# Optimization experiments

Hardware: AMD Instinct MI355X
Metric: run time of the kernel (lower is better)

Reference implementation:

```python
import jax, jax.numpy as jnp
import numpy as np

N = 100000      # nodes
E = 1600000     # edges
G = 1024        # graphs in batch
H = 128         # graph_hidden
F_IN = 38
DEPTH = 4
EPS = 1e-5


def setup_inputs() -> dict:
    key = jax.random.key(0)
    ks = jax.random.split(key, 16)
    inp = {
        "h": jax.random.normal(ks[0], (N, F_IN), jnp.float32),
        "src": jax.random.randint(ks[1], (E,), 0, N, jnp.int32),
        "dst": jax.random.randint(ks[2], (E,), 0, N, jnp.int32),
        "node2graph": jnp.sort(jax.random.randint(ks[3], (N,), 0, G, jnp.int32)),
        "W1": jax.random.normal(ks[4], (F_IN, H), jnp.float32) * 0.1,
        "b1": jnp.zeros((H,), jnp.float32),
        "g1": jnp.ones((H,), jnp.float32),
        "be1": jnp.zeros((H,), jnp.float32),
        "W2s": jax.random.normal(ks[5], (DEPTH - 1, H, H), jnp.float32) * 0.1,
        "b2s": jnp.zeros((DEPTH - 1, H), jnp.float32),
        "g2s": jnp.ones((DEPTH - 1, H), jnp.float32),
        "be2s": jnp.zeros((DEPTH - 1, H), jnp.float32),
        "aw": jax.random.normal(ks[6], (H, 1), jnp.float32) * 0.1,
        "ab": jnp.zeros((1,), jnp.float32),
        "Wf1": jax.random.normal(ks[7], (H, 512), jnp.float32) * 0.1,
        "bf1": jnp.zeros((512,), jnp.float32),
        "gf1": jnp.ones((512,), jnp.float32),
        "bef1": jnp.zeros((512,), jnp.float32),
        "Wl": jax.random.normal(ks[8], (512, 256), jnp.float32) * 0.05,
        "bl": jnp.zeros((256,), jnp.float32),
        "gl": jnp.ones((256,), jnp.float32),
        "bel": jnp.zeros((256,), jnp.float32),
        "Wf2": jax.random.normal(ks[9], (256, 67), jnp.float32) * 0.05,
        "bf2": jnp.zeros((67,), jnp.float32),
    }
    return inp


def _bn(x, g, b):
    # BatchNorm1d in training mode: batch stats (biased variance), eps=1e-5.
    m = jnp.mean(x, axis=0)
    v = jnp.mean(jnp.square(x - m), axis=0)
    return g * (x - m) * jax.lax.rsqrt(v + EPS) + b


def reference(h, src, dst, node2graph,
              W1, b1, g1, be1, W2s, b2s, g2s, be2s,
              aw, ab, Wf1, bf1, gf1, bef1, Wl, bl, gl, bel, Wf2, bf2):
    ones_e = jnp.ones((E,), h.dtype)
    deg_out = jax.ops.segment_sum(ones_e, src, num_segments=N)
    deg_in = jax.ops.segment_sum(ones_e, dst, num_segments=N)
    ns = jax.lax.rsqrt(jnp.maximum(deg_out, 1.0))  # src-side D^{-1/2}
    nd = jax.lax.rsqrt(jnp.maximum(deg_in, 1.0))   # dst-side D^{-1/2}

    def gconv(x, W, b):
        # DGL GraphConv norm='both': D_dst^{-1/2} A D_src^{-1/2} x W + b
        msg = (x * ns[:, None])[src]                      # [E, F] gather
        agg = jax.ops.segment_sum(msg, dst, num_segments=N)
        return (agg * nd[:, None]) @ W + b

    # dropout p = 0.0 -> identity
    x = jax.nn.relu(_bn(gconv(h, W1, b1), g1, be1))
    for i in range(DEPTH - 1):
        x = jax.nn.relu(_bn(gconv(x, W2s[i], b2s[i]), g2s[i], be2s[i]))

    # WeightAndSum readout: sigmoid-gated segment sum over nodes per graph
    atom_weights = x @ aw + ab                            # [N, 1] (pre-sigmoid, returned)
    w = jax.nn.sigmoid(atom_weights)
    hg = jax.ops.segment_sum(x * w, node2graph, num_segments=G)  # [G, H]

    y = jax.nn.relu(_bn(hg @ Wf1 + bf1, gf1, bef1))
    y = jax.nn.relu(_bn(y @ Wl + bl, gl, bel))
    y = jax.nn.sigmoid(y @ Wf2 + bf2)                     # [G, 67]
    return (y, atom_weights)
```

## Files before the change

### kernel.cpp

```cpp
#include <hip/hip_runtime.h>
#include <math.h>

#define NN 100000
#define NE 1600000
#define NG 1024
#define MAXDEG 64
#define EPSB 1e-5f

#define NBUK 1563
#define NBLK 256
#define EPB  6250
#define FLAT (2*NBUK*NBLK)
#define NCH  ((FLAT + 1023)/1024)

typedef _Float16 h16;
typedef __attribute__((ext_vector_type(2))) _Float16 h16x2;
typedef __attribute__((ext_vector_type(4))) _Float16 h16x4;
typedef __attribute__((ext_vector_type(8))) _Float16 h16x8;
typedef __attribute__((ext_vector_type(4))) float f32x4;

static __device__ __forceinline__ float sigmoidf_(float x){ return 1.f/(1.f+__expf(-x)); }

__global__ __launch_bounds__(512)
void k_hist(const int* __restrict__ src, const int* __restrict__ dst,
            int* __restrict__ blockHist){
  __shared__ int hd[NBUK];
  __shared__ int hs[NBUK];
  int b = blockIdx.x, t = threadIdx.x;
  for (int j = t; j < NBUK; j += 512){ hd[j] = 0; hs[j] = 0; }
  __syncthreads();
  int e0 = b*EPB, e1 = e0 + EPB;
  for (int i = e0 + t; i < e1; i += 512){
    atomicAdd(&hd[dst[i]>>6], 1);
    atomicAdd(&hs[src[i]>>6], 1);
  }
  __syncthreads();
  for (int j = t; j < NBUK; j += 512){
    blockHist[(size_t)j*NBLK + b] = hd[j];
    blockHist[(size_t)(NBUK + j)*NBLK + b] = hs[j];
  }
}

__global__ __launch_bounds__(256)
void k_scan1(int* __restrict__ data, int* __restrict__ csum){
  __shared__ int s[256];
  int blk = blockIdx.x, t = threadIdx.x;
  int base = blk*1024 + t*4;
  int v0=0,v1=0,v2=0,v3=0;
  if (base+0 < FLAT) v0 = data[base+0];
  if (base+1 < FLAT) v1 = data[base+1];
  if (base+2 < FLAT) v2 = data[base+2];
  if (base+3 < FLAT) v3 = data[base+3];
  int tot = v0+v1+v2+v3;
  s[t] = tot; __syncthreads();
  for (int o=1;o<256;o<<=1){ int x = (t>=o)? s[t-o]:0; __syncthreads(); s[t]+=x; __syncthreads(); }
  int excl = s[t] - tot;
  if (t == 255) csum[blk] = s[255];
  if (base+0 < FLAT) data[base+0] = excl;
  if (base+1 < FLAT) data[base+1] = excl + v0;
  if (base+2 < FLAT) data[base+2] = excl + v0 + v1;
  if (base+3 < FLAT) data[base+3] = excl + v0 + v1 + v2;
}

__global__ void k_scan2(int* __restrict__ csum){
  __shared__ int s[1024];
  int t = threadIdx.x;
  int x = (t < NCH) ? csum[t] : 0;
  s[t] = x; __syncthreads();
  for (int o=1;o<1024;o<<=1){ int y = (t>=o)? s[t-o]:0; __syncthreads(); s[t]+=y; __syncthreads(); }
  if (t < NCH) csum[t] = s[t] - x;
}

static __device__ __forceinline__ int rd_scanned(const int* data, const int* csum, int idx){
  return data[idx] + csum[idx >> 10];
}

__global__ __launch_bounds__(512)
void k_scatter(const int* __restrict__ src, const int* __restrict__ dst,
               const int* __restrict__ scanned, const int* __restrict__ csum,
               unsigned int* __restrict__ sortedBuf){
  __shared__ int bd[NBUK];
  __shared__ int bs[NBUK];
  int b = blockIdx.x, t = threadIdx.x;
  for (int j = t; j < NBUK; j += 512){
    bd[j] = rd_scanned(scanned, csum, j*NBLK + b);
    bs[j] = rd_scanned(scanned, csum, (NBUK + j)*NBLK + b);
  }
  __syncthreads();
  int e0 = b*EPB, e1 = e0 + EPB;
  for (int i = e0 + t; i < e1; i += 512){
    int s = src[i], d = dst[i];
    int posD = atomicAdd(&bd[d>>6], 1);
    sortedBuf[posD] = (unsigned int)s | ((unsigned int)(d & 63) << 20);
    int posS = atomicAdd(&bs[s>>6], 1);
    sortedBuf[posS] = (unsigned int)s;
  }
}

__global__ __launch_bounds__(256)
void k_build(const unsigned int* __restrict__ sortedBuf, const int* __restrict__ scanned,
             const int* __restrict__ csum, const float* __restrict__ h,
             int* __restrict__ eidx, int* __restrict__ degI,
             h16* __restrict__ nsh, float* __restrict__ nd, h16* __restrict__ hn){
  __shared__ int cnt[64];
  __shared__ float nsl[64];
  int k = blockIdx.x, t = threadIdx.x;
  int v0 = k*64;
  int nv = NN - v0; if (nv > 64) nv = 64;
  if (t < 64) cnt[t] = 0;
  __syncthreads();
  int startD = rd_scanned(scanned, csum, k*NBLK);
  int endD   = rd_scanned(scanned, csum, (k+1)*NBLK);
  for (int i = startD + t; i < endD; i += 256){
    unsigned int u = sortedBuf[i];
    int lid = (int)(u >> 20);
    int slot = atomicAdd(&cnt[lid], 1);
    if (slot < MAXDEG) eidx[(size_t)(v0 + lid)*MAXDEG + slot] = (int)(u & 0xFFFFFu);
  }
  __syncthreads();
  if (t < nv){
    int v = v0 + t;
    int dI = cnt[t];
    degI[v] = dI;
    nd[v] = rsqrtf(fmaxf((float)dI, 1.f));
    int c = dI > MAXDEG ? MAXDEG : dI;
    int ad = (c + 7) & ~7; if (ad < 8) ad = 8; if (ad > MAXDEG) ad = MAXDEG;
    for (int i = c; i < ad; i++) eidx[(size_t)v*MAXDEG + i] = NN;
  }
  __syncthreads();
  if (t < 64) cnt[t] = 0;
  __syncthreads();
  int startS = rd_scanned(scanned, csum, (NBUK + k)*NBLK);
  int endS   = (k+1 < NBUK) ? rd_scanned(scanned, csum, (NBUK + k + 1)*NBLK) : 2*NE;
  for (int i = startS + t; i < endS; i += 256){
    atomicAdd(&cnt[sortedBuf[i] & 63u], 1);
  }
  __syncthreads();
  if (t < 64){
    float nsv = 0.f;
    if (t < nv){
      nsv = rsqrtf(fmaxf((float)cnt[t], 1.f));
      nsh[v0 + t] = (h16)nsv;
    }
    nsl[t] = nsv;
  }
  __syncthreads();
  for (int i = t; i < 64*64; i += 256){
    int r = i >> 6, c = i & 63;
    int v = v0 + r;
    if (v < NN){
      float val = (c < 38) ? h[(size_t)v*38 + c]*nsl[r] : 0.f;
      hn[(size_t)v*64 + c] = (h16)val;
    }
  }
  if (k == 0){
    for (int i = t; i < 64; i += 256) hn[(size_t)NN*64 + i] = (h16)0.f;
  }
}

__global__ void k_prepg(const int* __restrict__ n2g,
                        int* __restrict__ gs, int* __restrict__ ge, float* __restrict__ stats,
                        h16* __restrict__ nsh, h16* __restrict__ XA, h16* __restrict__ XB){
  int v = blockIdx.x*256 + threadIdx.x;
  if (v < NN){
    int g = n2g[v];
    if (v == 0){
      for (int q = 0; q <= g; q++) gs[q] = 0;
      for (int q = 0; q < g; q++) ge[q] = 0;
    } else {
      int gp = n2g[v-1];
      if (gp != g){
        for (int q = gp+1; q <= g; q++) gs[q] = v;
        for (int q = gp; q < g; q++) ge[q] = v;
      }
    }
    if (v == NN-1){
      for (int q = g+1; q < NG; q++) gs[q] = NN;
      for (int q = g; q < NG; q++) ge[q] = NN;
    }
  }
  if (v == NN) nsh[NN] = (h16)0.f;
  if (blockIdx.x == 0){
    int t = threadIdx.x;
    for (int j = t; j < 4096; j += 256) stats[j] = 0.f;
    if (t < 128){ XA[(size_t)NN*128 + t] = (h16)0.f; XB[(size_t)NN*128 + t] = (h16)0.f; }
  }
}

__global__ void k_convall(const float* __restrict__ W1, const float* __restrict__ W2s,
                          const float* __restrict__ Wf1, const float* __restrict__ Wl,
                          h16* __restrict__ W1t, h16* __restrict__ W2t,
                          h16* __restrict__ Wf1t, h16* __restrict__ Wlt){
  int i = blockIdx.x*256 + threadIdx.x;
  if (i < 8192){
    int c = i >> 6, k = i & 63;
    W1t[i] = (k < 38) ? (h16)W1[(size_t)k*128 + c] : (h16)0.f;
  } else if (i < 57344){
    int j = i - 8192; int l = j >> 14; int r = j & 16383;
    int c = r >> 7, k = r & 127;
    W2t[j] = (h16)W2s[(size_t)l*16384 + (size_t)k*128 + c];
  } else if (i < 122880){
    int j = i - 57344; int c = j >> 7, k = j & 127;
    Wf1t[j] = (h16)Wf1[(size_t)k*512 + c];
  } else if (i < 253952){
    int j = i - 122880; int c = j >> 9, k = j & 511;
    Wlt[j] = (h16)Wl[(size_t)k*256 + c];
  }
}

__global__ __launch_bounds__(256)
void k_gs40(const h16* __restrict__ hn, const int* __restrict__ eidx,
            const int* __restrict__ degI, const float* __restrict__ nd,
            h16* __restrict__ A38){
  int v = (blockIdx.x*256 + threadIdx.x) >> 6;
  int lane = threadIdx.x & 63;
  if (v >= NN) return;
  int deg = degI[v]; if (deg > MAXDEG) deg = MAXDEG;
  int deg8 = (deg + 7) & ~7; if (deg8 < 8) deg8 = 8; if (deg8 > MAXDEG) deg8 = MAXDEG;
  const int* row = eidx + (size_t)v*MAXDEG;
  int g = lane / 20;
  int c0 = 2*(lane % 20);
  bool act = (lane < 40);
  int gg = g & 1;
  float a0 = 0.f, a1 = 0.f;
  int4 s4 = *(const int4*)(row + 4*gg);
  h16x2 u0={}, u1={}, u2={}, u3={};
  if (act){
    u0 = *(const h16x2*)(hn + (size_t)s4.x*64 + c0);
    u1 = *(const h16x2*)(hn + (size_t)s4.y*64 + c0);
    u2 = *(const h16x2*)(hn + (size_t)s4.z*64 + c0);
    u3 = *(const h16x2*)(hn + (size_t)s4.w*64 + c0);
  }
  for (int e = 0; e < deg8; e += 8){
    int nx = (e + 8 < deg8) ? e + 8 : e;
    int4 s4n = *(const int4*)(row + nx + 4*gg);
    h16x2 n0={}, n1={}, n2={}, n3={};
    if (act){
      n0 = *(const h16x2*)(hn + (size_t)s4n.x*64 + c0);
      n1 = *(const h16x2*)(hn + (size_t)s4n.y*64 + c0);
      n2 = *(const h16x2*)(hn + (size_t)s4n.z*64 + c0);
      n3 = *(const h16x2*)(hn + (size_t)s4n.w*64 + c0);
    }
    a0 += ((float)u0[0] + (float)u1[0]) + ((float)u2[0] + (float)u3[0]);
    a1 += ((float)u0[1] + (float)u1[1]) + ((float)u2[1] + (float)u3[1]);
    u0=n0; u1=n1; u2=n2; u3=n3;
  }
  float b0 = __shfl(a0, lane + 20);
  float b1 = __shfl(a1, lane + 20);
  if (lane < 20){
    float ndv = nd[v];
    h16x2 o; o[0] = (h16)((a0 + b0)*ndv); o[1] = (h16)((a1 + b1)*ndv);
    *(h16x2*)(A38 + (size_t)v*64 + c0) = o;
  } else if (lane < 32){
    h16x2 o; o[0] = (h16)0.f; o[1] = (h16)0.f;
    *(h16x2*)(A38 + (size_t)v*64 + 40 + 2*(lane - 20)) = o;
  }
}

__global__ __launch_bounds__(256)
void k_gs128(const h16* __restrict__ X, const int* __restrict__ eidx,
             const int* __restrict__ degI, const h16* __restrict__ nsh,
             const float* __restrict__ nd, const float* __restrict__ stats,
             const float* __restrict__ gam, const float* __restrict__ bet,
             h16* __restrict__ agg){
  __shared__ float scs[128], shs[128];
  int t = threadIdx.x;
  if (t < 128){
    float m = stats[t]*(1.f/(float)NN);
    float var = fmaxf(stats[128+t]*(1.f/(float)NN) - m*m, 0.f);
    float inv = rsqrtf(var + EPSB);
    float sc = gam[t]*inv;
    scs[t] = sc; shs[t] = fmaf(-sc, m, bet[t]);
  }
  __syncthreads();
  int v = (blockIdx.x*256 + t) >> 6;
  int lane = t & 63;
  if (v >= NN) return;
  int deg = degI[v]; if (deg > MAXDEG) deg = MAXDEG;
  int deg8 = (deg + 7) & ~7; if (deg8 < 8) deg8 = 8; if (deg8 > MAXDEG) deg8 = MAXDEG;
  const int* row = eidx + (size_t)v*MAXDEG;
  int half = lane >> 5;
  int c0 = 4*(lane & 31);
  h16x2 scp0, scp1, shp0, shp1, za;
  za[0] = (h16)0.f; za[1] = (h16)0.f;
  scp0[0]=(h16)scs[c0];   scp0[1]=(h16)scs[c0+1];
  scp1[0]=(h16)scs[c0+2]; scp1[1]=(h16)scs[c0+3];
  shp0[0]=(h16)shs[c0];   shp0[1]=(h16)shs[c0+1];
  shp1[0]=(h16)shs[c0+2]; shp1[1]=(h16)shs[c0+3];
  h16x2 acA0=za, acA1=za, acB0=za, acB1=za;
  int4 s4 = *(const int4*)(row + 4*half);
  h16 w0=nsh[s4.x], w1=nsh[s4.y], w2=nsh[s4.z], w3=nsh[s4.w];
  uint2 x0 = *(const uint2*)(X + (size_t)s4.x*128 + c0);
  uint2 x1 = *(const uint2*)(X + (size_t)s4.y*128 + c0);
  uint2 x2 = *(const uint2*)(X + (size_t)s4.z*128 + c0);
  uint2 x3 = *(const uint2*)(X + (size_t)s4.w*128 + c0);
  for (int e = 0; e < deg8; e += 8){
    int nx = (e + 8 < deg8) ? e + 8 : e;
    int4 s4n = *(const int4*)(row + nx + 4*half);
    h16 v0n=nsh[s4n.x], v1n=nsh[s4n.y], v2n=nsh[s4n.z], v3n=nsh[s4n.w];
    uint2 y0 = *(const uint2*)(X + (size_t)s4n.x*128 + c0);
    uint2 y1 = *(const uint2*)(X + (size_t)s4n.y*128 + c0);
    uint2 y2 = *(const uint2*)(X + (size_t)s4n.z*128 + c0);
    uint2 y3 = *(const uint2*)(X + (size_t)s4n.w*128 + c0);
    h16x2 np, pa, pb;
    np[0]=w0; np[1]=w0;
    pa = __builtin_bit_cast(h16x2, x0.x);
    pb = __builtin_bit_cast(h16x2, x0.y);
    pa = __builtin_elementwise_max(__builtin_elementwise_fma(pa, scp0, shp0), za);
    pb = __builtin_elementwise_max(__builtin_elementwise_fma(pb, scp1, shp1), za);
    acA0 = __builtin_elementwise_fma(pa, np, acA0);
    acA1 = __builtin_elementwise_fma(pb, np, acA1);
    np[0]=w1; np[1]=w1;
    pa = __builtin_bit_cast(h16x2, x1.x);
    pb = __builtin_bit_cast(h16x2, x1.y);
    pa = __builtin_elementwise_max(__builtin_elementwise_fma(pa, scp0, shp0), za);
    pb = __builtin_elementwise_max(__builtin_elementwise_fma(pb, scp1, shp1), za);
    acB0 = __builtin_elementwise_fma(pa, np, acB0);
    acB1 = __builtin_elementwise_fma(pb, np, acB1);
    np[0]=w2; np[1]=w2;
    pa = __builtin_bit_cast(h16x2, x2.x);
    pb = __builtin_bit_cast(h16x2, x2.y);
    pa = __builtin_elementwise_max(__builtin_elementwise_fma(pa, scp0, shp0), za);
    pb = __builtin_elementwise_max(__builtin_elementwise_fma(pb, scp1, shp1), za);
    acA0 = __builtin_elementwise_fma(pa, np, acA0);
    acA1 = __builtin_elementwise_fma(pb, np, acA1);
    np[0]=w3; np[1]=w3;
    pa = __builtin_bit_cast(h16x2, x3.x);
    pb = __builtin_bit_cast(h16x2, x3.y);
    pa = __builtin_elementwise_max(__builtin_elementwise_fma(pa, scp0, shp0), za);
    pb = __builtin_elementwise_max(__builtin_elementwise_fma(pb, scp1, shp1), za);
    acB0 = __builtin_elementwise_fma(pa, np, acB0);
    acB1 = __builtin_elementwise_fma(pb, np, acB1);
    x0=y0; x1=y1; x2=y2; x3=y3;
    w0=v0n; w1=v1n; w2=v2n; w3=v3n;
  }
  float a0 = (float)acA0[0] + (float)acB0[0];
  float a1 = (float)acA0[1] + (float)acB0[1];
  float a2 = (float)acA1[0] + (float)acB1[0];
  float a3 = (float)acA1[1] + (float)acB1[1];
  a0 += __shfl_xor(a0, 32);
  a1 += __shfl_xor(a1, 32);
  a2 += __shfl_xor(a2, 32);
  a3 += __shfl_xor(a3, 32);
  if (half == 0){
    float ndv = nd[v];
    h16x4 o;
    o[0] = (h16)(a0*ndv); o[1] = (h16)(a1*ndv);
    o[2] = (h16)(a2*ndv); o[3] = (h16)(a3*ndv);
    *(h16x4*)(agg + (size_t)v*128 + c0) = o;
  }
}

__global__ __launch_bounds__(256)
void k_mgemm(const h16* __restrict__ A, const h16* __restrict__ Wt,
             const float* __restrict__ bias, h16* __restrict__ Cout,
             float* __restrict__ stats, int M, int K, int Nc){
  __shared__ h16 As[128][72];
  __shared__ h16 Bs[128][72];
  __shared__ float sred[2][128];
  int m0 = blockIdx.x*128, n0 = blockIdx.y*128;
  int t = threadIdx.x, w = t>>6, lane = t&63;
  int wr = (w>>1)*64, wc = (w&1)*64;
  f32x4 acc[4][4] = {};

  int ar = t>>3;
  int ac = (t&7)*8;
  for (int k0=0; k0<K; k0+=64){
    #pragma unroll
    for (int rr=0; rr<128; rr+=32){
      int gm = m0 + ar + rr;
      h16x8 val = {};
      if (gm < M) val = *(const h16x8*)(A + (size_t)gm*K + k0 + ac);
      *(h16x8*)&As[ar+rr][ac] = val;
    }
    #pragma unroll
    for (int rr=0; rr<128; rr+=32){
      int gc = n0 + ar + rr;
      h16x8 val = {};
      if (gc < Nc) val = *(const h16x8*)(Wt + (size_t)gc*K + k0 + ac);
      *(h16x8*)&Bs[ar+rr][ac] = val;
    }
    __syncthreads();
    int rsel = lane & 15;
    #pragma unroll
    for (int kk=0; kk<64; kk+=32){
      int ksel = kk + (lane>>4)*8;
      h16x8 af[4], bfr[4];
      #pragma unroll
      for (int i=0;i<4;i++) af[i]  = *(const h16x8*)&As[wr + i*16 + rsel][ksel];
      #pragma unroll
      for (int j=0;j<4;j++) bfr[j] = *(const h16x8*)&Bs[wc + j*16 + rsel][ksel];
      #pragma unroll
      for (int i=0;i<4;i++)
        #pragma unroll
        for (int j=0;j<4;j++)
          acc[i][j] = __builtin_amdgcn_mfma_f32_16x16x32_f16(af[i], bfr[j], acc[i][j], 0, 0, 0);
    }
    __syncthreads();
  }

  float csum[4] = {}, csq[4] = {};
  int colsel = lane & 15, rowsel = (lane>>4)*4;
  #pragma unroll
  for (int j=0;j<4;j++){
    int gc = n0 + wc + j*16 + colsel;
    float bv = (gc < Nc) ? bias[gc] : 0.f;
    #pragma unroll
    for (int i=0;i<4;i++){
      #pragma unroll
      for (int r=0;r<4;r++){
        int gm = m0 + wr + i*16 + rowsel + r;
        if (gm < M && gc < Nc){
          float v = acc[i][j][r] + bv;
          Cout[(size_t)gm*Nc + gc] = (h16)v;
          csum[j] += v; csq[j] += v*v;
        }
      }
    }
  }
  if (stats){
    ((float*)sred)[t] = 0.f;
    __syncthreads();
    #pragma unroll
    for (int j=0;j<4;j++){
      int lc = wc + j*16 + colsel;
      atomicAdd(&sred[0][lc], csum[j]);
      atomicAdd(&sred[1][lc], csq[j]);
    }
    __syncthreads();
    if (t < 128){
      int gc = n0 + t;
      if (gc < Nc){
        atomicAdd(&stats[gc],      sred[0][t]);
        atomicAdd(&stats[Nc + gc], sred[1][t]);
      }
    }
  }
}

__global__ __launch_bounds__(256)
void k_mgemmbn(const h16* __restrict__ A, const h16* __restrict__ Wt,
               const float* __restrict__ bias, h16* __restrict__ Cout,
               float* __restrict__ statsOut, const float* __restrict__ statsIn,
               const float* __restrict__ gam, const float* __restrict__ bet,
               float invM, int M, int K, int Nc){
  __shared__ float scs[512], shs[512];
  __shared__ h16 As[128][72];
  __shared__ h16 Bs[128][72];
  __shared__ float sred[2][128];
  int t = threadIdx.x;
  for (int c = t; c < K; c += 256){
    float m = statsIn[c]*invM;
    float var = fmaxf(statsIn[K+c]*invM - m*m, 0.f);
    float inv = rsqrtf(var + EPSB);
    float sc = gam[c]*inv;
    scs[c] = sc; shs[c] = fmaf(-sc, m, bet[c]);
  }
  __syncthreads();
  int m0 = blockIdx.x*128, n0 = blockIdx.y*128;
  int w = t>>6, lane = t&63;
  int wr = (w>>1)*64, wc = (w&1)*64;
  f32x4 acc[4][4] = {};

  int ar = t>>3;
  int ac = (t&7)*8;
  for (int k0=0; k0<K; k0+=64){
    #pragma unroll
    for (int rr=0; rr<128; rr+=32){
      int gm = m0 + ar + rr;
      h16x8 val = {};
      if (gm < M){
        h16x8 raw = *(const h16x8*)(A + (size_t)gm*K + k0 + ac);
        #pragma unroll
        for (int j=0;j<8;j++){
          int kk = k0 + ac + j;
          val[j] = (h16)fmaxf(fmaf((float)raw[j], scs[kk], shs[kk]), 0.f);
        }
      }
      *(h16x8*)&As[ar+rr][ac] = val;
    }
    #pragma unroll
    for (int rr=0; rr<128; rr+=32){
      int gc = n0 + ar + rr;
      h16x8 val = {};
      if (gc < Nc) val = *(const h16x8*)(Wt + (size_t)gc*K + k0 + ac);
      *(h16x8*)&Bs[ar+rr][ac] = val;
    }
    __syncthreads();
    int rsel = lane & 15;
    #pragma unroll
    for (int kk=0; kk<64; kk+=32){
      int ksel = kk + (lane>>4)*8;
      h16x8 af[4], bfr[4];
      #pragma unroll
      for (int i=0;i<4;i++) af[i]  = *(const h16x8*)&As[wr + i*16 + rsel][ksel];
      #pragma unroll
      for (int j=0;j<4;j++) bfr[j] = *(const h16x8*)&Bs[wc + j*16 + rsel][ksel];
      #pragma unroll
      for (int i=0;i<4;i++)
        #pragma unroll
        for (int j=0;j<4;j++)
          acc[i][j] = __builtin_amdgcn_mfma_f32_16x16x32_f16(af[i], bfr[j], acc[i][j], 0, 0, 0);
    }
    __syncthreads();
  }

  float csum[4] = {}, csq[4] = {};
  int colsel = lane & 15, rowsel = (lane>>4)*4;
  #pragma unroll
  for (int j=0;j<4;j++){
    int gc = n0 + wc + j*16 + colsel;
    float bv = (gc < Nc) ? bias[gc] : 0.f;
    #pragma unroll
    for (int i=0;i<4;i++){
      #pragma unroll
      for (int r=0;r<4;r++){
        int gm = m0 + wr + i*16 + rowsel + r;
        if (gm < M && gc < Nc){
          float v = acc[i][j][r] + bv;
          Cout[(size_t)gm*Nc + gc] = (h16)v;
          csum[j] += v; csq[j] += v*v;
        }
      }
    }
  }
  ((float*)sred)[t] = 0.f;
  __syncthreads();
  #pragma unroll
  for (int j=0;j<4;j++){
    int lc = wc + j*16 + colsel;
    atomicAdd(&sred[0][lc], csum[j]);
    atomicAdd(&sred[1][lc], csq[j]);
  }
  __syncthreads();
  if (t < 128){
    int gc = n0 + t;
    if (gc < Nc){
      atomicAdd(&statsOut[gc],      sred[0][t]);
      atomicAdd(&statsOut[Nc + gc], sred[1][t]);
    }
  }
}

__global__ __launch_bounds__(256)
void k_readout(const h16* __restrict__ X, const float* __restrict__ stats,
               const float* __restrict__ gam, const float* __restrict__ bet,
               const float* __restrict__ aw, const float* __restrict__ ab,
               const int* __restrict__ gs, const int* __restrict__ ge,
               float* __restrict__ awout, h16* __restrict__ hg){
  __shared__ float scs[128], shs[128], awv[128];
  __shared__ float red[4][128];
  int t = threadIdx.x;
  if (t < 128){
    float m = stats[t]*(1.f/(float)NN);
    float var = fmaxf(stats[128+t]*(1.f/(float)NN) - m*m, 0.f);
    float inv = rsqrtf(var + EPSB);
    float sc = gam[t]*inv;
    scs[t] = sc; shs[t] = fmaf(-sc, m, bet[t]);
    awv[t] = aw[t];
  }
  __syncthreads();
  int g = blockIdx.x;
  int s = gs[g], e = ge[g];
  int w = t>>6, lane = t&63, c0 = 2*lane;
  float sc0=scs[c0], sc1=scs[c0+1], sh0=shs[c0], sh1=shs[c0+1];
  float aw0=awv[c0], aw1=awv[c0+1];
  float ab0 = ab[0];
  float acc0=0.f, acc1=0.f;
  for (int n = s + w; n < e; n += 4){
    h16x2 u = *(const h16x2*)(X + (size_t)n*128 + c0);
    float x0 = fmaxf(fmaf((float)u[0], sc0, sh0), 0.f);
    float x1 = fmaxf(fmaf((float)u[1], sc1, sh1), 0.f);
    float d = x0*aw0 + x1*aw1;
    #pragma unroll
    for (int o=32;o>0;o>>=1) d += __shfl_xor(d, o);
    float tv = d + ab0;
    if (lane == 0) awout[n] = tv;
    float wn = sigmoidf_(tv);
    acc0 = fmaf(x0, wn, acc0);
    acc1 = fmaf(x1, wn, acc1);
  }
  red[w][c0] = acc0; red[w][c0+1] = acc1;
  __syncthreads();
  if (w == 0){
    float a0 = red[0][c0] + red[1][c0] + red[2][c0] + red[3][c0];
    float a1 = red[0][c0+1] + red[1][c0+1] + red[2][c0+1] + red[3][c0+1];
    h16x2 o; o[0] = (h16)a0; o[1] = (h16)a1;
    *(h16x2*)(hg + (size_t)g*128 + c0) = o;
  }
}

__global__ __launch_bounds__(256)
void k_finalbn(const h16* __restrict__ y2p, const float* __restrict__ Wf2,
               const float* __restrict__ bf2v, const float* __restrict__ statsIn,
               const float* __restrict__ gam, const float* __restrict__ bet,
               float* __restrict__ out){
  __shared__ float scs[256], shs[256];
  int t = threadIdx.x;
  {
    float m = statsIn[t]*(1.f/(float)NG);
    float var = fmaxf(statsIn[256+t]*(1.f/(float)NG) - m*m, 0.f);
    float inv = rsqrtf(var + EPSB);
    float sc = gam[t]*inv;
    scs[t] = sc; shs[t] = fmaf(-sc, m, bet[t]);
  }
  __syncthreads();
  int idx = blockIdx.x*256 + t;
  if (idx >= NG*67) return;
  int g = idx / 67, c = idx % 67;
  float s = bf2v[c];
  const h16* row = y2p + (size_t)g*256;
  for (int k=0;k<256;k+=2){
    h16x2 u = *(const h16x2*)(row + k);
    float x0 = fmaxf(fmaf((float)u[0], scs[k],   shs[k]),   0.f);
    float x1 = fmaxf(fmaf((float)u[1], scs[k+1], shs[k+1]), 0.f);
    s = fmaf(x0, Wf2[(size_t)k*67 + c], s);
    s = fmaf(x1, Wf2[(size_t)(k+1)*67 + c], s);
  }
  out[(size_t)g*67 + c] = sigmoidf_(s);
}

extern "C" void kernel_launch(void* const* d_in, const int* in_sizes, int n_in,
                              void* d_out, int out_size, void* d_ws, size_t ws_size,
                              hipStream_t stream){
  const float* h   = (const float*)d_in[0];
  const int*   src = (const int*)d_in[1];
  const int*   dst = (const int*)d_in[2];
  const int*   n2g = (const int*)d_in[3];
  const float* W1  = (const float*)d_in[4];
  const float* b1  = (const float*)d_in[5];
  const float* g1  = (const float*)d_in[6];
  const float* be1 = (const float*)d_in[7];
  const float* W2s = (const float*)d_in[8];
  const float* b2s = (const float*)d_in[9];
  const float* g2s = (const float*)d_in[10];
  const float* be2s= (const float*)d_in[11];
  const float* aw  = (const float*)d_in[12];
  const float* ab  = (const float*)d_in[13];
  const float* Wf1 = (const float*)d_in[14];
  const float* bf1 = (const float*)d_in[15];
  const float* gf1 = (const float*)d_in[16];
  const float* bef1= (const float*)d_in[17];
  const float* Wl  = (const float*)d_in[18];
  const float* bl  = (const float*)d_in[19];
  const float* gl  = (const float*)d_in[20];
  const float* bel = (const float*)d_in[21];
  const float* Wf2 = (const float*)d_in[22];
  const float* bf2v= (const float*)d_in[23];
  float* out = (float*)d_out;

  char* p = (char*)d_ws;
  auto carve = [&](size_t bytes)->void*{
    void* r = (void*)p; p += (bytes + 255) & ~(size_t)255; return r;
  };
  h16* XA   = (h16*)carve((size_t)(NN+1)*128*2);
  h16* XB   = (h16*)carve((size_t)(NN+1)*128*2);
  h16* hn   = (h16*)carve((size_t)(NN+1)*64*2);
  h16* A38  = (h16*)carve((size_t)NN*64*2);
  int* eidx = (int*)carve((size_t)NN*MAXDEG*4);
  unsigned int* sortedBuf = (unsigned int*)carve((size_t)2*NE*4);
  int* blockHist = (int*)carve((size_t)FLAT*4);
  int* csum = (int*)carve(1024*4);
  int* degI = (int*)carve((size_t)NN*4);
  h16* nsh = (h16*)carve((size_t)(NN+1)*2);
  float* nd = (float*)carve((size_t)NN*4);
  int* gsge = (int*)carve((size_t)2*NG*4);
  h16* hg   = (h16*)carve((size_t)NG*128*2);
  h16* y1p  = (h16*)carve((size_t)NG*512*2);
  h16* y2p  = (h16*)carve((size_t)NG*256*2);
  float* stats = (float*)carve(4096*4);
  h16* W1t  = (h16*)carve((size_t)128*64*2);
  h16* W2t  = (h16*)carve((size_t)3*128*128*2);
  h16* Wf1t = (h16*)carve((size_t)512*128*2);
  h16* Wlt  = (h16*)carve((size_t)256*512*2);

  int* gs = gsge;
  int* ge = gsge + NG;
  float* st1  = stats;
  float* st2a = stats + 256;
  float* st2b = stats + 512;
  float* st2c = stats + 768;
  float* stf1 = stats + 1024;
  float* stl  = stats + 2048;
  float* st2[3] = { st2a, st2b, st2c };

  k_convall<<<(253952+255)/256, 256, 0, stream>>>(W1, W2s, Wf1, Wl, W1t, W2t, Wf1t, Wlt);
  k_prepg  <<<(NN+1+255)/256, 256, 0, stream>>>(n2g, gs, ge, stats, nsh, XA, XB);

  k_hist   <<<NBLK, 512, 0, stream>>>(src, dst, blockHist);
  k_scan1  <<<NCH, 256, 0, stream>>>(blockHist, csum);
  k_scan2  <<<1, 1024, 0, stream>>>(csum);
  k_scatter<<<NBLK, 512, 0, stream>>>(src, dst, blockHist, csum, sortedBuf);
  k_build  <<<NBUK, 256, 0, stream>>>(sortedBuf, blockHist, csum, h, eidx, degI, nsh, nd, hn);

  const int nodeBlocks = (NN + 3)/4;
  const int gemmBlocks = (NN + 127)/128;

  k_gs40 <<<nodeBlocks, 256, 0, stream>>>(hn, eidx, degI, nd, A38);
  k_mgemm<<<dim3(gemmBlocks,1), 256, 0, stream>>>(A38, W1t, b1, XA, st1, NN, 64, 128);

  const float* stPrev[3] = { st1, st2a, st2b };
  const float* gPrev[3]  = { g1, g2s, g2s + 128 };
  const float* bePrev[3] = { be1, be2s, be2s + 128 };
  for (int i=0;i<3;i++){
    k_gs128<<<nodeBlocks, 256, 0, stream>>>(XA, eidx, degI, nsh, nd,
                                            stPrev[i], gPrev[i], bePrev[i], XB);
    k_mgemm<<<dim3(gemmBlocks,1), 256, 0, stream>>>(XB, W2t + (size_t)i*128*128, b2s + i*128,
                                                    XA, st2[i], NN, 128, 128);
  }

  k_readout<<<NG, 256, 0, stream>>>(XA, st2c, g2s + 256, be2s + 256, aw, ab,
                                    gs, ge, out + (size_t)NG*67, hg);

  k_mgemm  <<<dim3(NG/128, 4), 256, 0, stream>>>(hg, Wf1t, bf1, y1p, stf1, NG, 128, 512);
  k_mgemmbn<<<dim3(NG/128, 2), 256, 0, stream>>>(y1p, Wlt, bl, y2p, stl, stf1, gf1, bef1,
                                                 1.0f/(float)NG, NG, 512, 256);
  k_finalbn<<<(NG*67+255)/256, 256, 0, stream>>>(y2p, Wf2, bf2v, stl, gl, bel, out);
}
```

Measured before the change: 647.2 us.

## Load GEMM A-fragments directly from global memory and merge init kernels

The MFMA GEMM kernels (plain and BN-fused) stop staging the A tile in shared memory. Each wave now loads its A fragments straight from global memory into registers, applying the BN affine and ReLU per fragment in the fused variant, while only the weight tile still goes through LDS. The aim is to remove an LDS round trip and shared-memory footprint for A, which is used by a single wave anyway. The trade-off is less coalesced global loads and possibly redundant loads across the wave pairs that share rows. Separately, the weight-conversion and graph-prep kernels are merged into one launch to save a kernel launch.

Measured after the change: 634.8 us. About the same (-1.9%).

```diff
diff --git a/kernel.cpp b/kernel.cpp
--- a/kernel.cpp
+++ b/kernel.cpp
@@ -158,39 +158,13 @@
   }
 }
 
-__global__ void k_prepg(const int* __restrict__ n2g,
-                        int* __restrict__ gs, int* __restrict__ ge, float* __restrict__ stats,
-                        h16* __restrict__ nsh, h16* __restrict__ XA, h16* __restrict__ XB){
-  int v = blockIdx.x*256 + threadIdx.x;
-  if (v < NN){
-    int g = n2g[v];
-    if (v == 0){
-      for (int q = 0; q <= g; q++) gs[q] = 0;
-      for (int q = 0; q < g; q++) ge[q] = 0;
-    } else {
-      int gp = n2g[v-1];
-      if (gp != g){
-        for (int q = gp+1; q <= g; q++) gs[q] = v;
-        for (int q = gp; q < g; q++) ge[q] = v;
-      }
-    }
-    if (v == NN-1){
-      for (int q = g+1; q < NG; q++) gs[q] = NN;
-      for (int q = g; q < NG; q++) ge[q] = NN;
-    }
-  }
-  if (v == NN) nsh[NN] = (h16)0.f;
-  if (blockIdx.x == 0){
-    int t = threadIdx.x;
-    for (int j = t; j < 4096; j += 256) stats[j] = 0.f;
-    if (t < 128){ XA[(size_t)NN*128 + t] = (h16)0.f; XB[(size_t)NN*128 + t] = (h16)0.f; }
-  }
-}
-
-__global__ void k_convall(const float* __restrict__ W1, const float* __restrict__ W2s,
-                          const float* __restrict__ Wf1, const float* __restrict__ Wl,
-                          h16* __restrict__ W1t, h16* __restrict__ W2t,
-                          h16* __restrict__ Wf1t, h16* __restrict__ Wlt){
+__global__ void k_init(const float* __restrict__ W1, const float* __restrict__ W2s,
+                       const float* __restrict__ Wf1, const float* __restrict__ Wl,
+                       h16* __restrict__ W1t, h16* __restrict__ W2t,
+                       h16* __restrict__ Wf1t, h16* __restrict__ Wlt,
+                       const int* __restrict__ n2g, int* __restrict__ gs, int* __restrict__ ge,
+                       float* __restrict__ stats, h16* __restrict__ nsh,
+                       h16* __restrict__ XA, h16* __restrict__ XB){
   int i = blockIdx.x*256 + threadIdx.x;
   if (i < 8192){
     int c = i >> 6, k = i & 63;
@@ -205,6 +179,30 @@
   } else if (i < 253952){
     int j = i - 122880; int c = j >> 9, k = j & 511;
     Wlt[j] = (h16)Wl[(size_t)k*256 + c];
+  }
+  int v = i;
+  if (v < NN){
+    int g = n2g[v];
+    if (v == 0){
+      for (int q = 0; q <= g; q++) gs[q] = 0;
+      for (int q = 0; q < g; q++) ge[q] = 0;
+    } else {
+      int gp = n2g[v-1];
+      if (gp != g){
+        for (int q = gp+1; q <= g; q++) gs[q] = v;
+        for (int q = gp; q < g; q++) ge[q] = v;
+      }
+    }
+    if (v == NN-1){
+      for (int q = g+1; q < NG; q++) gs[q] = NN;
+      for (int q = g; q < NG; q++) ge[q] = NN;
+    }
+  }
+  if (v == NN) nsh[NN] = (h16)0.f;
+  if (blockIdx.x == 0){
+    int t = threadIdx.x;
+    for (int j = t; j < 4096; j += 256) stats[j] = 0.f;
+    if (t < 128){ XA[(size_t)NN*128 + t] = (h16)0.f; XB[(size_t)NN*128 + t] = (h16)0.f; }
   }
 }
 
@@ -355,41 +353,42 @@
 void k_mgemm(const h16* __restrict__ A, const h16* __restrict__ Wt,
              const float* __restrict__ bias, h16* __restrict__ Cout,
              float* __restrict__ stats, int M, int K, int Nc){
-  __shared__ h16 As[128][72];
   __shared__ h16 Bs[128][72];
   __shared__ float sred[2][128];
   int m0 = blockIdx.x*128, n0 = blockIdx.y*128;
   int t = threadIdx.x, w = t>>6, lane = t&63;
   int wr = (w>>1)*64, wc = (w&1)*64;
+  int rsel = lane & 15;
+  int kblk = (lane>>4)*8;
   f32x4 acc[4][4] = {};
-
-  int ar = t>>3;
-  int ac = (t&7)*8;
+  const h16x8 zero8 = {};
   for (int k0=0; k0<K; k0+=64){
-    #pragma unroll
-    for (int rr=0; rr<128; rr+=32){
-      int gm = m0 + ar + rr;
-      h16x8 val = {};
-      if (gm < M) val = *(const h16x8*)(A + (size_t)gm*K + k0 + ac);
-      *(h16x8*)&As[ar+rr][ac] = val;
-    }
-    #pragma unroll
-    for (int rr=0; rr<128; rr+=32){
-      int gc = n0 + ar + rr;
-      h16x8 val = {};
-      if (gc < Nc) val = *(const h16x8*)(Wt + (size_t)gc*K + k0 + ac);
-      *(h16x8*)&Bs[ar+rr][ac] = val;
+    {
+      int br = t>>1;
+      int bc = (t&1)*32;
+      int gc = n0 + br;
+      if (gc < Nc){
+        const h16* wp = Wt + (size_t)gc*K + k0 + bc;
+        #pragma unroll
+        for (int j=0;j<4;j++)
+          *(h16x8*)&Bs[br][bc + j*8] = *(const h16x8*)(wp + j*8);
+      } else {
+        #pragma unroll
+        for (int j=0;j<4;j++)
+          *(h16x8*)&Bs[br][bc + j*8] = zero8;
+      }
     }
     __syncthreads();
-    int rsel = lane & 15;
     #pragma unroll
     for (int kk=0; kk<64; kk+=32){
-      int ksel = kk + (lane>>4)*8;
       h16x8 af[4], bfr[4];
       #pragma unroll
-      for (int i=0;i<4;i++) af[i]  = *(const h16x8*)&As[wr + i*16 + rsel][ksel];
+      for (int i=0;i<4;i++){
+        int gm = m0 + wr + i*16 + rsel;
+        af[i] = (gm < M) ? *(const h16x8*)(A + (size_t)gm*K + k0 + kk + kblk) : zero8;
+      }
       #pragma unroll
-      for (int j=0;j<4;j++) bfr[j] = *(const h16x8*)&Bs[wc + j*16 + rsel][ksel];
+      for (int j=0;j<4;j++) bfr[j] = *(const h16x8*)&Bs[wc + j*16 + rsel][kk + kblk];
       #pragma unroll
       for (int i=0;i<4;i++)
         #pragma unroll
@@ -445,7 +444,6 @@
                const float* __restrict__ gam, const float* __restrict__ bet,
                float invM, int M, int K, int Nc){
   __shared__ float scs[512], shs[512];
-  __shared__ h16 As[128][72];
   __shared__ h16 Bs[128][72];
   __shared__ float sred[2][128];
   int t = threadIdx.x;
@@ -460,42 +458,46 @@
   int m0 = blockIdx.x*128, n0 = blockIdx.y*128;
   int w = t>>6, lane = t&63;
   int wr = (w>>1)*64, wc = (w&1)*64;
+  int rsel = lane & 15;
+  int kblk = (lane>>4)*8;
   f32x4 acc[4][4] = {};
-
-  int ar = t>>3;
-  int ac = (t&7)*8;
+  const h16x8 zero8 = {};
   for (int k0=0; k0<K; k0+=64){
-    #pragma unroll
-    for (int rr=0; rr<128; rr+=32){
-      int gm = m0 + ar + rr;
-      h16x8 val = {};
-      if (gm < M){
-        h16x8 raw = *(const h16x8*)(A + (size_t)gm*K + k0 + ac);
+    {
+      int br = t>>1;
+      int bc = (t&1)*32;
+      int gc = n0 + br;
+      if (gc < Nc){
+        const h16* wp = Wt + (size_t)gc*K + k0 + bc;
         #pragma unroll
-        for (int j=0;j<8;j++){
-          int kk = k0 + ac + j;
-          val[j] = (h16)fmaxf(fmaf((float)raw[j], scs[kk], shs[kk]), 0.f);
-        }
+        for (int j=0;j<4;j++)
+          *(h16x8*)&Bs[br][bc + j*8] = *(const h16x8*)(wp + j*8);
+      } else {
+        #pragma unroll
+        for (int j=0;j<4;j++)
+          *(h16x8*)&Bs[br][bc + j*8] = zero8;
       }
-      *(h16x8*)&As[ar+rr][ac] = val;
-    }
-    #pragma unroll
-    for (int rr=0; rr<128; rr+=32){
-      int gc = n0 + ar + rr;
-      h16x8 val = {};
-      if (gc < Nc) val = *(const h16x8*)(Wt + (size_t)gc*K + k0 + ac);
-      *(h16x8*)&Bs[ar+rr][ac] = val;
     }
     __syncthreads();
-    int rsel = lane & 15;
     #pragma unroll
     for (int kk=0; kk<64; kk+=32){
-      int ksel = kk + (lane>>4)*8;
       h16x8 af[4], bfr[4];
       #pragma unroll
-      for (int i=0;i<4;i++) af[i]  = *(const h16x8*)&As[wr + i*16 + rsel][ksel];
+      for (int i=0;i<4;i++){
+        int gm = m0 + wr + i*16 + rsel;
+        h16x8 val = zero8;
+        if (gm < M){
+          h16x8 raw = *(const h16x8*)(A + (size_t)gm*K + k0 + kk + kblk);
+          #pragma unroll
+          for (int j=0;j<8;j++){
+            int c = k0 + kk + kblk + j;
+            val[j] = (h16)fmaxf(fmaf((float)raw[j], scs[c], shs[c]), 0.f);
+          }
+        }
+        af[i] = val;
+      }
       #pragma unroll
-      for (int j=0;j<4;j++) bfr[j] = *(const h16x8*)&Bs[wc + j*16 + rsel][ksel];
+      for (int j=0;j<4;j++) bfr[j] = *(const h16x8*)&Bs[wc + j*16 + rsel][kk + kblk];
       #pragma unroll
       for (int i=0;i<4;i++)
         #pragma unroll
@@ -684,8 +686,8 @@
   float* stl  = stats + 2048;
   float* st2[3] = { st2a, st2b, st2c };
 
-  k_convall<<<(253952+255)/256, 256, 0, stream>>>(W1, W2s, Wf1, Wl, W1t, W2t, Wf1t, Wlt);
-  k_prepg  <<<(NN+1+255)/256, 256, 0, stream>>>(n2g, gs, ge, stats, nsh, XA, XB);
+  k_init<<<(253952+255)/256, 256, 0, stream>>>(W1, W2s, Wf1, Wl, W1t, W2t, Wf1t, Wlt,
+                                               n2g, gs, ge, stats, nsh, XA, XB);
 
   k_hist   <<<NBLK, 512, 0, stream>>>(src, dst, blockHist);
   k_scan1  <<<NCH, 256, 0, stream>>>(blockHist, csum);
```
